# Kernel optimization log

Measured on AMD Instinct MI355X. Metric: run time of the kernel, lower is better.

## Reference

```python
import jax, jax.numpy as jnp
import numpy as np

N = 100000
DROPOUT = 0.5


def gcn_conv(x, row, col, W, b, n):
    # PyG GCNConv: out = D^-1/2 (A+I) D^-1/2 (x W) + b
    # self-loops already appended to (row, col) by caller via add_self_loops
    w = jnp.ones(row.shape[0], dtype=x.dtype)
    deg = jax.ops.segment_sum(w, col, num_segments=n)
    dinv = jnp.where(deg > 0, jax.lax.rsqrt(deg), 0.0)
    norm = dinv[row] * dinv[col]  # [E]
    xw = x @ W  # [N, out]
    msg = norm[:, None] * xw[row]  # gather sources
    out = jax.ops.segment_sum(msg, col, num_segments=n)  # scatter-add to targets
    return out + b


def add_self_loops(edge_index, n):
    loop = jnp.arange(n, dtype=edge_index.dtype)
    row = jnp.concatenate([edge_index[0], loop])
    col = jnp.concatenate([edge_index[1], loop])
    return row, col


def setup_inputs() -> dict:
    key = jax.random.key(0)
    k1, k2, k3, k4 = jax.random.split(key, 4)
    x = jax.random.normal(k1, (N, 512), dtype=jnp.float32)
    edge_index = jax.random.randint(k2, (2, 3200000), 0, N, dtype=jnp.int32)
    W1 = jax.random.normal(k3, (512, 16), dtype=jnp.float32) * (1.0 / np.sqrt(512))
    b1 = jnp.zeros((16,), dtype=jnp.float32)
    W2 = jax.random.normal(k4, (16, 40), dtype=jnp.float32) * (1.0 / np.sqrt(16))
    b2 = jnp.zeros((40,), dtype=jnp.float32)
    return {"x": x, "edge_index": edge_index, "W1": W1, "b1": b1, "W2": W2, "b2": b2}


def reference(x, edge_index, W1, b1, W2, b2):
    n = x.shape[0]
    row, col = add_self_loops(edge_index, n)
    h = gcn_conv(x, row, col, W1, b1, n)  # [N, 16]
    # dropout (training mode) with fixed key for determinism
    keep = jax.random.bernoulli(jax.random.key(42), 1.0 - DROPOUT, h.shape)
    h = jnp.where(keep, h / (1.0 - DROPOUT), 0.0)
    out = gcn_conv(h, row, col, W2, b2, n)  # [N, 40]
    return out
```

## Files before the change

kernel.cpp:

```cpp
#include <hip/hip_runtime.h>
#include <cstdint>


#define TFR(R) { x0 += x1; x1 = (x1 << (R)) | (x1 >> (32 - (R))); x1 ^= x0; }

__device__ __forceinline__ void tf2x32(uint32_t k0, uint32_t k1,
                                       uint32_t c0, uint32_t c1,
                                       uint32_t& o0, uint32_t& o1) {
    const uint32_t kx = k0 ^ k1 ^ 0x1BD11BDAu;
    uint32_t x0 = c0 + k0, x1 = c1 + k1;
    TFR(13) TFR(15) TFR(26) TFR(6)   x0 += k1; x1 += kx + 1u;
    TFR(17) TFR(29) TFR(16) TFR(24)  x0 += kx; x1 += k0 + 2u;
    TFR(13) TFR(15) TFR(26) TFR(6)   x0 += k0; x1 += k1 + 3u;
    TFR(17) TFR(29) TFR(16) TFR(24)  x0 += k1; x1 += kx + 4u;
    TFR(13) TFR(15) TFR(26) TFR(6)   x0 += kx; x1 += k0 + 5u;
    o0 = x0; o1 = x1;
}

#define NIL 0xFFFFFFFFu

__global__ void k_init(uint32_t* __restrict__ head, int N, uint32_t* __restrict__ kat) {
    int i = blockIdx.x * blockDim.x + threadIdx.x;
    if (i < N) head[i] = NIL;
    if (i == 0) {
        uint32_t o0, o1;
        tf2x32(0u, 0u, 0u, 0u, o0, o1);
        *kat = (o0 == 0x6b200159u && o1 == 0x99ba4efeu) ? 1u : 0u;
    }
}

__global__ void k_build(const int* __restrict__ row, const int* __restrict__ col,
                        uint32_t* __restrict__ head, uint2* __restrict__ packed, int E) {
    int e = blockIdx.x * blockDim.x + threadIdx.x;
    if (e >= E) return;
    uint32_t r = (uint32_t)row[e];
    int c = col[e];
    uint32_t old = atomicExch(&head[c], (uint32_t)e);
    packed[e] = make_uint2(r, old);
}

__global__ void k_walk(const uint32_t* __restrict__ head, const uint2* __restrict__ packed,
                       float* __restrict__ dinv, int N) {
    int n = blockIdx.x * blockDim.x + threadIdx.x;
    if (n >= N) return;
    uint32_t e = head[n];
    int cnt = 0;
    while (e != NIL) { cnt++; e = packed[e].y; }
    dinv[n] = rsqrtf(1.0f + (float)cnt);
}

__global__ __launch_bounds__(256) void k_mm1(
    const float* __restrict__ x, const float* __restrict__ W1,
    const float* __restrict__ dinv, float* __restrict__ y1, int N) {
    int n = blockIdx.x * blockDim.x + threadIdx.x;
    if (n >= N) return;
    float acc[16];
#pragma unroll
    for (int f = 0; f < 16; ++f) acc[f] = 0.0f;
    const float4* xr = reinterpret_cast<const float4*>(x + (size_t)n * 512);
#pragma unroll 4
    for (int j = 0; j < 128; ++j) {
        float4 xv = xr[j];
        const float* w = W1 + j * 64;
#pragma unroll
        for (int f = 0; f < 16; ++f)
            acc[f] += xv.x * w[f] + xv.y * w[16 + f] + xv.z * w[32 + f] + xv.w * w[48 + f];
    }
    float dv = dinv[n];
    float* yo = y1 + (size_t)n * 16;
#pragma unroll
    for (int f = 0; f < 16; ++f) yo[f] = dv * acc[f];
}

__global__ __launch_bounds__(256) void k_gather16(
    const uint32_t* __restrict__ head, const uint2* __restrict__ packed,
    const float* __restrict__ dinv, const float* __restrict__ y,
    float* __restrict__ agg, int N) {
    int t = blockIdx.x * 256 + threadIdx.x;
    int c = t >> 2;
    int j = t & 3;
    if (c >= N) return;
    float4 acc = *reinterpret_cast<const float4*>(y + (size_t)c * 16 + j * 4);
    uint32_t e = head[c];
    while (e != NIL) {
        uint2 p = packed[e];
        const float4 v = *reinterpret_cast<const float4*>(y + (size_t)p.x * 16 + j * 4);
        acc.x += v.x; acc.y += v.y; acc.z += v.z; acc.w += v.w;
        e = p.y;
    }
    float dc = dinv[c];
    float4 o = make_float4(dc * acc.x, dc * acc.y, dc * acc.z, dc * acc.w);
    *reinterpret_cast<float4*>(agg + (size_t)c * 16 + j * 4) = o;
}

__global__ void k_finalize(const float* __restrict__ agg1, const float* __restrict__ b1,
                           const float* __restrict__ dinv, float* __restrict__ y2,
                           int N, const uint32_t* __restrict__ kat) {
    int i = blockIdx.x * blockDim.x + threadIdx.x;
    if (i >= N * 16) return;
    int n = i >> 4;
    int f = i & 15;
    uint32_t o0, o1;
    tf2x32(0u, 42u, 0u, (uint32_t)i, o0, o1);
    uint32_t bits = o0 ^ o1;
    float hv = (bits & 0x80000000u) ? 0.0f : (agg1[i] + b1[f]) * 2.0f;
    if (*kat == 0u) hv = 0.0f;
    y2[i] = dinv[n] * hv;
}

__global__ __launch_bounds__(256) void k_mm2(
    const float* __restrict__ agg2, const float* __restrict__ W2,
    const float* __restrict__ b2, float* __restrict__ out, int N) {
    int n = blockIdx.x * blockDim.x + threadIdx.x;
    if (n >= N) return;
    float a[16];
    const float4* s = reinterpret_cast<const float4*>(agg2 + (size_t)n * 16);
#pragma unroll
    for (int j = 0; j < 4; ++j) {
        float4 v = s[j];
        a[4 * j + 0] = v.x; a[4 * j + 1] = v.y; a[4 * j + 2] = v.z; a[4 * j + 3] = v.w;
    }
    float acc[40];
#pragma unroll
    for (int f = 0; f < 40; ++f) acc[f] = b2[f];
#pragma unroll
    for (int k = 0; k < 16; ++k) {
        float av = a[k];
        const float* w = W2 + k * 40;
#pragma unroll
        for (int f = 0; f < 40; ++f) acc[f] += av * w[f];
    }
    float* o = out + (size_t)n * 40;
#pragma unroll
    for (int f = 0; f < 40; ++f) o[f] = acc[f];
}

extern "C" void kernel_launch(void* const* d_in, const int* in_sizes, int n_in,
                              void* d_out, int out_size, void* d_ws, size_t ws_size,
                              hipStream_t stream) {
    const float* x  = (const float*)d_in[0];
    const int*   ei = (const int*)d_in[1];
    const float* W1 = (const float*)d_in[2];
    const float* b1 = (const float*)d_in[3];
    const float* W2 = (const float*)d_in[4];
    const float* b2 = (const float*)d_in[5];
    float* out = (float*)d_out;

    const int E = in_sizes[1] / 2;
    const int N = in_sizes[0] / 512;
    const int* row = ei;
    const int* col = ei + E;

    uint32_t* head   = (uint32_t*)d_ws;
    float*    dinv   = (float*)(head + N);
    uint2*    packed = (uint2*)(dinv + N);
    float*    aggbuf = (float*)(packed + E);
    uint32_t* kat    = (uint32_t*)(aggbuf + (size_t)16 * N);

    float* ybuf = (float*)d_out;

    dim3 blk(256);
    dim3 gN((N + 255) / 256);
    dim3 gE((E + 255) / 256);
    dim3 gNF((N * 16 + 255) / 256);
    dim3 gN4((N * 4 + 255) / 256);

    k_init<<<gN, blk, 0, stream>>>(head, N, kat);
    k_build<<<gE, blk, 0, stream>>>(row, col, head, packed, E);
    k_walk<<<gN, blk, 0, stream>>>(head, packed, dinv, N);
    k_mm1<<<gN, blk, 0, stream>>>(x, W1, dinv, ybuf , N);
    k_gather16<<<gN4, blk, 0, stream>>>(head, packed, dinv, ybuf, aggbuf, N);
    k_finalize<<<gNF, blk, 0, stream>>>(aggbuf, b1, dinv, ybuf , N, kat);
    k_gather16<<<gN4, blk, 0, stream>>>(head, packed, dinv, ybuf, aggbuf, N);
    k_mm2<<<gN, blk, 0, stream>>>(aggbuf, W2, b2, out, N);
}
```

Before: 715.2 us.

## Tile first matmul through shared memory and fuse gathers with dropout and second matmul

The first projection now stages W1 and transposed 128-row tiles of x in shared memory, so each thread computes a 2x4 output block with coalesced loads instead of walking one 2 KB row on its own. The first gather is fused with bias, dropout and normalisation, and the second gather is fused with the 16x40 output projection through a shared-memory tile. Together these drop two launches and the round trips of an intermediate N x 16 buffer. In exchange the matmul kernel uses about 65 KB of shared memory per block, which may limit occupancy.

```diff
diff --git a/kernel.cpp b/kernel.cpp
--- a/kernel.cpp
+++ b/kernel.cpp
@@ -52,87 +52,150 @@
 __global__ __launch_bounds__(256) void k_mm1(
     const float* __restrict__ x, const float* __restrict__ W1,
     const float* __restrict__ dinv, float* __restrict__ y1, int N) {
-    int n = blockIdx.x * blockDim.x + threadIdx.x;
-    if (n >= N) return;
-    float acc[16];
-#pragma unroll
-    for (int f = 0; f < 16; ++f) acc[f] = 0.0f;
-    const float4* xr = reinterpret_cast<const float4*>(x + (size_t)n * 512);
+    __shared__ float Ws[512 * 16];
+    __shared__ float Xs[64 * 129];
+    const int tid = threadIdx.x;
+    const int row0 = blockIdx.x * 128;
+
+    {
+        const float4* w4 = reinterpret_cast<const float4*>(W1);
+        float4* s4 = reinterpret_cast<float4*>(Ws);
+#pragma unroll
+        for (int i = 0; i < 8; ++i) s4[tid + i * 256] = w4[tid + i * 256];
+    }
+
+    const int rq = tid & 63;
+    const int fq = tid >> 6;
+    float acc0[4] = {0.f, 0.f, 0.f, 0.f};
+    float acc1[4] = {0.f, 0.f, 0.f, 0.f};
+
+    for (int kt = 0; kt < 8; ++kt) {
+        __syncthreads();
+#pragma unroll
+        for (int i = 0; i < 8; ++i) {
+            int idx = tid + i * 256;
+            int r = idx >> 4;
+            int c4 = idx & 15;
+            int grow = row0 + r;
+            float4 v = make_float4(0.f, 0.f, 0.f, 0.f);
+            if (grow < N)
+                v = *reinterpret_cast<const float4*>(x + (size_t)grow * 512 + kt * 64 + c4 * 4);
+            int kb = 4 * c4;
+            Xs[(kb + 0) * 129 + r] = v.x;
+            Xs[(kb + 1) * 129 + r] = v.y;
+            Xs[(kb + 2) * 129 + r] = v.z;
+            Xs[(kb + 3) * 129 + r] = v.w;
+        }
+        __syncthreads();
+        const float4* wv4 = reinterpret_cast<const float4*>(Ws) + (size_t)kt * 64 * 4 + fq;
 #pragma unroll 4
-    for (int j = 0; j < 128; ++j) {
-        float4 xv = xr[j];
-        const float* w = W1 + j * 64;
-#pragma unroll
-        for (int f = 0; f < 16; ++f)
-            acc[f] += xv.x * w[f] + xv.y * w[16 + f] + xv.z * w[32 + f] + xv.w * w[48 + f];
-    }
-    float dv = dinv[n];
-    float* yo = y1 + (size_t)n * 16;
-#pragma unroll
-    for (int f = 0; f < 16; ++f) yo[f] = dv * acc[f];
-}
-
-__global__ __launch_bounds__(256) void k_gather16(
+        for (int k = 0; k < 64; ++k) {
+            float xv0 = Xs[k * 129 + rq];
+            float xv1 = Xs[k * 129 + rq + 64];
+            float4 wv = wv4[k * 4];
+            acc0[0] += xv0 * wv.x; acc0[1] += xv0 * wv.y;
+            acc0[2] += xv0 * wv.z; acc0[3] += xv0 * wv.w;
+            acc1[0] += xv1 * wv.x; acc1[1] += xv1 * wv.y;
+            acc1[2] += xv1 * wv.z; acc1[3] += xv1 * wv.w;
+        }
+    }
+    int r0 = row0 + rq, r1 = r0 + 64;
+    if (r0 < N) {
+        float dv = dinv[r0];
+        float4 o = make_float4(dv * acc0[0], dv * acc0[1], dv * acc0[2], dv * acc0[3]);
+        *reinterpret_cast<float4*>(y1 + (size_t)r0 * 16 + fq * 4) = o;
+    }
+    if (r1 < N) {
+        float dv = dinv[r1];
+        float4 o = make_float4(dv * acc1[0], dv * acc1[1], dv * acc1[2], dv * acc1[3]);
+        *reinterpret_cast<float4*>(y1 + (size_t)r1 * 16 + fq * 4) = o;
+    }
+}
+
+__global__ __launch_bounds__(256) void k_gather_fin(
     const uint32_t* __restrict__ head, const uint2* __restrict__ packed,
-    const float* __restrict__ dinv, const float* __restrict__ y,
-    float* __restrict__ agg, int N) {
+    const float* __restrict__ dinv, const float* __restrict__ b1,
+    const float* __restrict__ y1, float* __restrict__ y2, int N,
+    const uint32_t* __restrict__ kat) {
     int t = blockIdx.x * 256 + threadIdx.x;
     int c = t >> 2;
     int j = t & 3;
     if (c >= N) return;
-    float4 acc = *reinterpret_cast<const float4*>(y + (size_t)c * 16 + j * 4);
+    float4 acc = *reinterpret_cast<const float4*>(y1 + (size_t)c * 16 + j * 4);
     uint32_t e = head[c];
     while (e != NIL) {
         uint2 p = packed[e];
-        const float4 v = *reinterpret_cast<const float4*>(y + (size_t)p.x * 16 + j * 4);
+        const float4 v = *reinterpret_cast<const float4*>(y1 + (size_t)p.x * 16 + j * 4);
         acc.x += v.x; acc.y += v.y; acc.z += v.z; acc.w += v.w;
         e = p.y;
     }
     float dc = dinv[c];
-    float4 o = make_float4(dc * acc.x, dc * acc.y, dc * acc.z, dc * acc.w);
-    *reinterpret_cast<float4*>(agg + (size_t)c * 16 + j * 4) = o;
-}
-
-__global__ void k_finalize(const float* __restrict__ agg1, const float* __restrict__ b1,
-                           const float* __restrict__ dinv, float* __restrict__ y2,
-                           int N, const uint32_t* __restrict__ kat) {
-    int i = blockIdx.x * blockDim.x + threadIdx.x;
-    if (i >= N * 16) return;
-    int n = i >> 4;
-    int f = i & 15;
-    uint32_t o0, o1;
-    tf2x32(0u, 42u, 0u, (uint32_t)i, o0, o1);
-    uint32_t bits = o0 ^ o1;
-    float hv = (bits & 0x80000000u) ? 0.0f : (agg1[i] + b1[f]) * 2.0f;
-    if (*kat == 0u) hv = 0.0f;
-    y2[i] = dinv[n] * hv;
-}
-
-__global__ __launch_bounds__(256) void k_mm2(
-    const float* __restrict__ agg2, const float* __restrict__ W2,
-    const float* __restrict__ b2, float* __restrict__ out, int N) {
-    int n = blockIdx.x * blockDim.x + threadIdx.x;
-    if (n >= N) return;
-    float a[16];
-    const float4* s = reinterpret_cast<const float4*>(agg2 + (size_t)n * 16);
-#pragma unroll
-    for (int j = 0; j < 4; ++j) {
-        float4 v = s[j];
-        a[4 * j + 0] = v.x; a[4 * j + 1] = v.y; a[4 * j + 2] = v.z; a[4 * j + 3] = v.w;
-    }
-    float acc[40];
-#pragma unroll
-    for (int f = 0; f < 40; ++f) acc[f] = b2[f];
-#pragma unroll
-    for (int k = 0; k < 16; ++k) {
-        float av = a[k];
-        const float* w = W2 + k * 40;
-#pragma unroll
-        for (int f = 0; f < 40; ++f) acc[f] += av * w[f];
-    }
-    float* o = out + (size_t)n * 40;
-#pragma unroll
-    for (int f = 0; f < 40; ++f) o[f] = acc[f];
+    float4 bv = *reinterpret_cast<const float4*>(b1 + 4 * j);
+    float ag[4] = {dc * acc.x + bv.x, dc * acc.y + bv.y,
+                   dc * acc.z + bv.z, dc * acc.w + bv.w};
+    uint32_t ok = *kat;
+    float o[4];
+#pragma unroll
+    for (int ii = 0; ii < 4; ++ii) {
+        uint32_t idx = (uint32_t)c * 16u + (uint32_t)(4 * j + ii);
+        uint32_t o0, o1;
+        tf2x32(0u, 42u, 0u, idx, o0, o1);
+        uint32_t bits = o0 ^ o1;
+        float hv = (bits & 0x80000000u) ? 0.0f : ag[ii] * 2.0f;
+        if (ok == 0u) hv = 0.0f;
+        o[ii] = dc * hv;
+    }
+    *reinterpret_cast<float4*>(y2 + (size_t)c * 16 + 4 * j) =
+        make_float4(o[0], o[1], o[2], o[3]);
+}
+
+__global__ __launch_bounds__(256) void k_gather_mm2(
+    const uint32_t* __restrict__ head, const uint2* __restrict__ packed,
+    const float* __restrict__ dinv, const float* __restrict__ y2,
+    const float* __restrict__ W2, const float* __restrict__ b2,
+    float* __restrict__ out, int N) {
+    __shared__ float W2s[16 * 40];
+    __shared__ float b2s[40];
+    __shared__ float aggS[64 * 17];
+    const int tid = threadIdx.x;
+    for (int i = tid; i < 640; i += 256) W2s[i] = W2[i];
+    if (tid < 40) b2s[tid] = b2[tid];
+    const int cl = tid >> 2;
+    const int j = tid & 3;
+    const int c = blockIdx.x * 64 + cl;
+    if (c < N) {
+        float4 acc = *reinterpret_cast<const float4*>(y2 + (size_t)c * 16 + j * 4);
+        uint32_t e = head[c];
+        while (e != NIL) {
+            uint2 p = packed[e];
+            const float4 v = *reinterpret_cast<const float4*>(y2 + (size_t)p.x * 16 + j * 4);
+            acc.x += v.x; acc.y += v.y; acc.z += v.z; acc.w += v.w;
+            e = p.y;
+        }
+        float dc = dinv[c];
+        aggS[cl * 17 + 4 * j + 0] = dc * acc.x;
+        aggS[cl * 17 + 4 * j + 1] = dc * acc.y;
+        aggS[cl * 17 + 4 * j + 2] = dc * acc.z;
+        aggS[cl * 17 + 4 * j + 3] = dc * acc.w;
+    }
+    __syncthreads();
+    if (c < N) {
+        float a[16];
+#pragma unroll
+        for (int k = 0; k < 16; ++k) a[k] = aggS[cl * 17 + k];
+        float o[10];
+#pragma unroll
+        for (int m = 0; m < 10; ++m) o[m] = b2s[j * 10 + m];
+#pragma unroll
+        for (int k = 0; k < 16; ++k) {
+            float av = a[k];
+#pragma unroll
+            for (int m = 0; m < 10; ++m) o[m] += av * W2s[k * 40 + j * 10 + m];
+        }
+        float* op = out + (size_t)c * 40 + j * 10;
+#pragma unroll
+        for (int m = 0; m < 10; ++m) op[m] = o[m];
+    }
 }
 
 extern "C" void kernel_launch(void* const* d_in, const int* in_sizes, int n_in,
@@ -151,26 +214,24 @@
     const int* row = ei;
     const int* col = ei + E;
 
-    uint32_t* head   = (uint32_t*)d_ws;
-    float*    dinv   = (float*)(head + N);
+    uint32_t* head = (uint32_t*)d_ws;
+    float*    dinv = (float*)(head + N);
     uint2*    packed = (uint2*)(dinv + N);
-    float*    aggbuf = (float*)(packed + E);
-    uint32_t* kat    = (uint32_t*)(aggbuf + (size_t)16 * N);
-
-    float* ybuf = (float*)d_out;
+    float*    y2   = (float*)(packed + E);
+    uint32_t* kat  = (uint32_t*)(y2 + (size_t)16 * N);
+
+    float* y1 = (float*)d_out;
 
     dim3 blk(256);
     dim3 gN((N + 255) / 256);
     dim3 gE((E + 255) / 256);
-    dim3 gNF((N * 16 + 255) / 256);
+    dim3 gMM((N + 127) / 128);
     dim3 gN4((N * 4 + 255) / 256);
 
     k_init<<<gN, blk, 0, stream>>>(head, N, kat);
     k_build<<<gE, blk, 0, stream>>>(row, col, head, packed, E);
     k_walk<<<gN, blk, 0, stream>>>(head, packed, dinv, N);
-    k_mm1<<<gN, blk, 0, stream>>>(x, W1, dinv, ybuf , N);
-    k_gather16<<<gN4, blk, 0, stream>>>(head, packed, dinv, ybuf, aggbuf, N);
-    k_finalize<<<gNF, blk, 0, stream>>>(aggbuf, b1, dinv, ybuf , N, kat);
-    k_gather16<<<gN4, blk, 0, stream>>>(head, packed, dinv, ybuf, aggbuf, N);
-    k_mm2<<<gN, blk, 0, stream>>>(aggbuf, W2, b2, out, N);
-}
+    k_mm1<<<gMM, blk, 0, stream>>>(x, W1, dinv, y1, N);
+    k_gather_fin<<<gN4, blk, 0, stream>>>(head, packed, dinv, b1, y1, y2, N, kat);
+    k_gather_mm2<<<gN4, blk, 0, stream>>>(head, packed, dinv, y2, W2, b2, out, N);
+}
```

Result: no change. 719.7 us (+0.6%).
